# Performance work log

Measured on AMD Instinct MI355X. Metric: run time of the kernel, lower is better.

## Reference

```python
import jax, jax.numpy as jnp
import numpy as np


def setup_inputs() -> dict:
    key = jax.random.key(0)
    k1, k2, k3, k4, k5 = jax.random.split(key, 5)
    B_, S, D_in, D_out, R = 2, 2048, 4096, 4096, 4
    return {
        "x": jax.random.normal(k1, (B_, S, D_in), dtype=jnp.float32),
        "weight": jax.random.normal(k2, (D_out, D_in), dtype=jnp.float32) * 0.02,
        "bias": jax.random.normal(k3, (D_out,), dtype=jnp.float32) * 0.02,
        "scale_A": jax.random.normal(k4, (D_out, R), dtype=jnp.float32),
        "scale_B": jax.random.normal(k5, (R, D_in), dtype=jnp.float32),
        "rank_magnitude": jnp.ones((R,), dtype=jnp.float32),
    }


def reference(x, weight, bias, scale_A, scale_B, rank_magnitude):
    # Factored forward with default bound_mode='tanh', A_max=B_max=1.0, pad=0:
    #   y = sum_k g_k * A[:, k] * ((x * B[k]) @ Q.T) + bias
    Q = weight  # snapped_mode=None, _Q=None -> Q = raw weight
    A = jnp.tanh(scale_A)            # [O, R]
    Bm = jnp.tanh(scale_B)           # [R, I] (pad == 0)
    Ag = A * rank_magnitude[None, :]  # fold g_k into A -> [O, R]
    # [b,s,i] x [r,i] -> [b,s,r,i]; contract i with Q [o,i]; weight by Ag [o,r]
    y = jnp.einsum("bsi,ri,oi,or->bso", x, Bm, Q, Ag)
    return y + bias
```

## Files before the change

kernel.cpp:

```cpp
#include <hip/hip_runtime.h>
#include <hip/hip_bf16.h>

typedef __attribute__((ext_vector_type(8))) short bf16x8;
typedef __attribute__((ext_vector_type(4))) float f32x4;
typedef __attribute__((ext_vector_type(4))) short s16x4;

#define M_DIM 4096
#define N_DIM 4096
#define K_DIM 4096
#define R_DIM 4

__device__ __forceinline__ short to_bf16(float f) {
    __hip_bfloat16 h = __float2bfloat16(f);
    return *reinterpret_cast<short*>(&h);
}

__global__ __launch_bounds__(256)
void k_prep(const float* __restrict__ sA, const float* __restrict__ sB,
            const float* __restrict__ g, float* __restrict__ tB,
            float* __restrict__ tAg) {
    int i = blockIdx.x * 256 + threadIdx.x;
    if (i < R_DIM * K_DIM) {
        tB[i] = tanhf(sB[i]);
    } else {
        int j = i - R_DIM * K_DIM;
        tAg[j] = tanhf(sA[j]) * g[j & 3];
    }
}

__global__ __launch_bounds__(256)
void k_xcast(const float* __restrict__ x, __hip_bfloat16* __restrict__ xb) {
    const size_t i = ((size_t)blockIdx.x * 256 + threadIdx.x) << 3;
    float4 u = *(const float4*)&x[i];
    float4 v = *(const float4*)&x[i + 4];
    bf16x8 pk;
    pk[0] = to_bf16(u.x); pk[1] = to_bf16(u.y);
    pk[2] = to_bf16(u.z); pk[3] = to_bf16(u.w);
    pk[4] = to_bf16(v.x); pk[5] = to_bf16(v.y);
    pk[6] = to_bf16(v.z); pk[7] = to_bf16(v.w);
    *(bf16x8*)&xb[i] = pk;
}

__global__ __launch_bounds__(256)
void k_weff(const float* __restrict__ w, const float* __restrict__ tB,
            const float* __restrict__ tAg, __hip_bfloat16* __restrict__ weff) {
    const int o = blockIdx.x;
    const float a0 = tAg[o * 4 + 0];
    const float a1 = tAg[o * 4 + 1];
    const float a2 = tAg[o * 4 + 2];
    const float a3 = tAg[o * 4 + 3];
#pragma unroll
    for (int it = 0; it < 4; ++it) {
        const int i = (it * 256 + (int)threadIdx.x) << 2;
        float4 wv = *(const float4*)&w[(size_t)o * K_DIM + i];
        float4 b0 = *(const float4*)&tB[0 * K_DIM + i];
        float4 b1 = *(const float4*)&tB[1 * K_DIM + i];
        float4 b2 = *(const float4*)&tB[2 * K_DIM + i];
        float4 b3 = *(const float4*)&tB[3 * K_DIM + i];
        float s0 = a0 * b0.x + a1 * b1.x + a2 * b2.x + a3 * b3.x;
        float s1 = a0 * b0.y + a1 * b1.y + a2 * b2.y + a3 * b3.y;
        float s2 = a0 * b0.z + a1 * b1.z + a2 * b2.z + a3 * b3.z;
        float s3 = a0 * b0.w + a1 * b1.w + a2 * b2.w + a3 * b3.w;
        s16x4 pk;
        pk[0] = to_bf16(wv.x * s0);
        pk[1] = to_bf16(wv.y * s1);
        pk[2] = to_bf16(wv.z * s2);
        pk[3] = to_bf16(wv.w * s3);
        *(s16x4*)&weff[(size_t)o * K_DIM + i] = pk;
    }
}

#define MFMA_N(q, n, bA, bB) \
    acc[2*(q)][(n)]   = __builtin_amdgcn_mfma_f32_16x16x32_bf16(a0, bA, acc[2*(q)][(n)],   0, 0, 0); \
    acc[2*(q)][(n)]   = __builtin_amdgcn_mfma_f32_16x16x32_bf16(a1, bB, acc[2*(q)][(n)],   0, 0, 0); \
    acc[2*(q)+1][(n)] = __builtin_amdgcn_mfma_f32_16x16x32_bf16(a2, bA, acc[2*(q)+1][(n)], 0, 0, 0); \
    acc[2*(q)+1][(n)] = __builtin_amdgcn_mfma_f32_16x16x32_bf16(a3, bB, acc[2*(q)+1][(n)], 0, 0, 0);

#define PHASE(d, q, STAGE_STMT, WAIT_STMT) \
    { \
        const int Ab = ((d) * 2 + wr) * 8192; \
        a0 = FRAG(Ab, (2*(q))   * 16 + l15, cb0); \
        a1 = FRAG(Ab, (2*(q))   * 16 + l15, cb1); \
        a2 = FRAG(Ab, (2*(q)+1) * 16 + l15, cb0); \
        a3 = FRAG(Ab, (2*(q)+1) * 16 + l15, cb1); \
        if ((q) == 0) { \
            const int Bb = 32768 + ((d) * 2 + (wc >> 1)) * 8192; \
            b0 = FRAG(Bb, br0, cb0); b1 = FRAG(Bb, br0, cb1); \
            b2 = FRAG(Bb, br1, cb0); b3 = FRAG(Bb, br1, cb1); \
            b4 = FRAG(Bb, br2, cb0); b5 = FRAG(Bb, br2, cb1); \
            b6 = FRAG(Bb, br3, cb0); b7 = FRAG(Bb, br3, cb1); \
        } \
        STAGE_STMT; \
        __builtin_amdgcn_s_barrier(); \
        asm volatile("s_waitcnt lgkmcnt(0)" ::: "memory"); \
        __builtin_amdgcn_sched_barrier(0); \
        __builtin_amdgcn_s_setprio(1); \
        MFMA_N(q, 0, b0, b1); MFMA_N(q, 1, b2, b3); \
        MFMA_N(q, 2, b4, b5); MFMA_N(q, 3, b6, b7); \
        __builtin_amdgcn_s_setprio(0); \
        WAIT_STMT; \
        __builtin_amdgcn_s_barrier(); \
    }

__global__ __launch_bounds__(512)
void k_gemm8(const __hip_bfloat16* __restrict__ xb,
             const __hip_bfloat16* __restrict__ weff,
             const float* __restrict__ bias, float* __restrict__ out) {
    __shared__ short lds[65536];

    const int tid  = threadIdx.x;
    const int lane = tid & 63;
    const int wid  = tid >> 6;
    const int wr   = wid >> 2;
    const int wc   = wid & 3;
    const int l15  = lane & 15;
    const int cb0  = (lane >> 4) << 4;
    const int cb1  = cb0 + 64;

    const int bid = blockIdx.x;
    const int swz = (bid & 7) * 32 + (bid >> 3);
    const int m0g = (swz >> 4) << 8;
    const int n0g = (swz & 15) << 8;

    const int br0 = (wc & 1) * 64 + 0  + l15;
    const int br1 = (wc & 1) * 64 + 16 + l15;
    const int br2 = (wc & 1) * 64 + 32 + l15;
    const int br3 = (wc & 1) * 64 + 48 + l15;

    auto STAGE = [&](const __hip_bfloat16* __restrict__ src, int gr0, int k0, int base) {
#pragma unroll
        for (int p = 0; p < 2; ++p) {
            const int P    = p * 8192 + tid * 16;
            const int row  = P >> 7;
            const int colb = (P & 127) ^ ((row & 7) << 4);
            const __hip_bfloat16* g = src + ((size_t)(gr0 + row) << 12) + (k0 + (colb >> 1));
            __builtin_amdgcn_global_load_lds(
                (const __attribute__((address_space(1))) void*)g,
                (__attribute__((address_space(3))) void*)&lds[base + (P >> 1)],
                16, 0, 0);
        }
    };

    auto FRAG = [&](int base, int row, int cb) -> bf16x8 {
        const int byte = ((((row << 7) + cb) ^ ((row & 7) << 4))) + base * 2;
        return *(const bf16x8*)((const char*)lds + byte);
    };

    f32x4 acc[8][4] = {};
    bf16x8 a0, a1, a2, a3, b0, b1, b2, b3, b4, b5, b6, b7;

    STAGE(xb,   m0g,       0,  0);
    STAGE(xb,   m0g + 128, 0,  8192);
    STAGE(weff, n0g,       0,  32768);
    STAGE(weff, n0g + 128, 0,  40960);
    STAGE(weff, n0g,       64, 49152);
    STAGE(weff, n0g + 128, 64, 57344);
    asm volatile("s_waitcnt vmcnt(4)" ::: "memory");
    __builtin_amdgcn_s_barrier();

    for (int i = 0; i < 32; ++i) {
        const int t1k = (2 * i + 1) * 64;
        const int kA  = (2 * i + 2 < 64 ? 2 * i + 2 : 63) * 64;
        const int kB  = (2 * i + 3 < 64 ? 2 * i + 3 : 63) * 64;

        PHASE(0, 0, STAGE(xb,   m0g,       t1k, 16384), );
        PHASE(0, 1, STAGE(xb,   m0g + 128, t1k, 24576), );
        PHASE(0, 2, STAGE(weff, n0g,       kA,  32768), );
        PHASE(0, 3, STAGE(weff, n0g + 128, kA,  40960),
              asm volatile("s_waitcnt vmcnt(4)" ::: "memory"));
        PHASE(1, 0, STAGE(xb,   m0g,       kA,  0), );
        PHASE(1, 1, STAGE(xb,   m0g + 128, kA,  8192), );
        PHASE(1, 2, STAGE(weff, n0g,       kB,  49152), );
        PHASE(1, 3, STAGE(weff, n0g + 128, kB,  57344),
              asm volatile("s_waitcnt vmcnt(4)" ::: "memory"));
    }

#pragma unroll
    for (int n = 0; n < 4; ++n) {
        const int col = n0g + wc * 64 + n * 16 + l15;
        const float bv = bias[col];
#pragma unroll
        for (int m = 0; m < 8; ++m) {
            const int rbase = m0g + wr * 128 + m * 16 + ((lane >> 4) << 2);
#pragma unroll
            for (int j = 0; j < 4; ++j)
                out[(size_t)(rbase + j) * N_DIM + col] = acc[m][n][j] + bv;
        }
    }
}

extern "C" void kernel_launch(void* const* d_in, const int* in_sizes, int n_in,
                              void* d_out, int out_size, void* d_ws, size_t ws_size,
                              hipStream_t stream) {
    const float* x    = (const float*)d_in[0];
    const float* w    = (const float*)d_in[1];
    const float* bias = (const float*)d_in[2];
    const float* sA   = (const float*)d_in[3];
    const float* sB   = (const float*)d_in[4];
    const float* g    = (const float*)d_in[5];
    float* out = (float*)d_out;

    __hip_bfloat16* weff = (__hip_bfloat16*)d_ws;
    __hip_bfloat16* xb   = (__hip_bfloat16*)((char*)d_ws + (32ull << 20));
    float* tB  = (float*)((char*)d_ws + (64ull << 20));
    float* tAg = (float*)((char*)d_ws + (64ull << 20) + (R_DIM * K_DIM * 4));

    k_prep<<<dim3((2 * R_DIM * K_DIM) / 256), dim3(256), 0, stream>>>(sA, sB, g, tB, tAg);
    k_xcast<<<dim3((M_DIM * K_DIM) / (256 * 8)), dim3(256), 0, stream>>>(x, xb);
    k_weff<<<dim3(N_DIM), dim3(256), 0, stream>>>(w, tB, tAg, weff);
    k_gemm8<<<dim3((M_DIM / 256) * (N_DIM / 256)), dim3(512), 0, stream>>>(xb, weff, bias, out);
}
```

Baseline: 156.2 us.

## Software-pipeline LDS fragment reads with MFMA using double-buffered A registers

Restructures the GEMM main loop so the A fragments for the next quarter-tile are read from LDS while the current quarter's MFMAs run, alternating between two register sets (x/y). B fragments are read once per half-iteration, and the explicit lgkmcnt waits and per-phase scheduling barriers are dropped so LDS latency can hide behind matrix math. It also adds a min-blocks-per-CU launch bound of 2. That bound tightens the register budget against 128 accumulator registers plus 16 fragment registers, which risks spilling, and LDS use of 128 KB per block may stop two blocks from sharing a CU anyway.

```diff
diff --git a/kernel.cpp b/kernel.cpp
--- a/kernel.cpp
+++ b/kernel.cpp
@@ -70,39 +70,71 @@
     }
 }
 
-#define MFMA_N(q, n, bA, bB) \
-    acc[2*(q)][(n)]   = __builtin_amdgcn_mfma_f32_16x16x32_bf16(a0, bA, acc[2*(q)][(n)],   0, 0, 0); \
-    acc[2*(q)][(n)]   = __builtin_amdgcn_mfma_f32_16x16x32_bf16(a1, bB, acc[2*(q)][(n)],   0, 0, 0); \
-    acc[2*(q)+1][(n)] = __builtin_amdgcn_mfma_f32_16x16x32_bf16(a2, bA, acc[2*(q)+1][(n)], 0, 0, 0); \
-    acc[2*(q)+1][(n)] = __builtin_amdgcn_mfma_f32_16x16x32_bf16(a3, bB, acc[2*(q)+1][(n)], 0, 0, 0);
-
-#define PHASE(d, q, STAGE_STMT, WAIT_STMT) \
-    { \
-        const int Ab = ((d) * 2 + wr) * 8192; \
-        a0 = FRAG(Ab, (2*(q))   * 16 + l15, cb0); \
-        a1 = FRAG(Ab, (2*(q))   * 16 + l15, cb1); \
-        a2 = FRAG(Ab, (2*(q)+1) * 16 + l15, cb0); \
-        a3 = FRAG(Ab, (2*(q)+1) * 16 + l15, cb1); \
-        if ((q) == 0) { \
-            const int Bb = 32768 + ((d) * 2 + (wc >> 1)) * 8192; \
-            b0 = FRAG(Bb, br0, cb0); b1 = FRAG(Bb, br0, cb1); \
-            b2 = FRAG(Bb, br1, cb0); b3 = FRAG(Bb, br1, cb1); \
-            b4 = FRAG(Bb, br2, cb0); b5 = FRAG(Bb, br2, cb1); \
-            b6 = FRAG(Bb, br3, cb0); b7 = FRAG(Bb, br3, cb1); \
-        } \
-        STAGE_STMT; \
-        __builtin_amdgcn_s_barrier(); \
-        asm volatile("s_waitcnt lgkmcnt(0)" ::: "memory"); \
-        __builtin_amdgcn_sched_barrier(0); \
-        __builtin_amdgcn_s_setprio(1); \
-        MFMA_N(q, 0, b0, b1); MFMA_N(q, 1, b2, b3); \
-        MFMA_N(q, 2, b4, b5); MFMA_N(q, 3, b6, b7); \
-        __builtin_amdgcn_s_setprio(0); \
-        WAIT_STMT; \
-        __builtin_amdgcn_s_barrier(); \
-    }
-
-__global__ __launch_bounds__(512)
+#define MFMA(A, B, C) __builtin_amdgcn_mfma_f32_16x16x32_bf16(A, B, C, 0, 0, 0)
+
+#define MFMA_Q(q, A0, A1, A2, A3) \
+    acc[2*(q)][0]   = MFMA(A0, b0, acc[2*(q)][0]); \
+    acc[2*(q)][0]   = MFMA(A1, b1, acc[2*(q)][0]); \
+    acc[2*(q)+1][0] = MFMA(A2, b0, acc[2*(q)+1][0]); \
+    acc[2*(q)+1][0] = MFMA(A3, b1, acc[2*(q)+1][0]); \
+    acc[2*(q)][1]   = MFMA(A0, b2, acc[2*(q)][1]); \
+    acc[2*(q)][1]   = MFMA(A1, b3, acc[2*(q)][1]); \
+    acc[2*(q)+1][1] = MFMA(A2, b2, acc[2*(q)+1][1]); \
+    acc[2*(q)+1][1] = MFMA(A3, b3, acc[2*(q)+1][1]); \
+    acc[2*(q)][2]   = MFMA(A0, b4, acc[2*(q)][2]); \
+    acc[2*(q)][2]   = MFMA(A1, b5, acc[2*(q)][2]); \
+    acc[2*(q)+1][2] = MFMA(A2, b4, acc[2*(q)+1][2]); \
+    acc[2*(q)+1][2] = MFMA(A3, b5, acc[2*(q)+1][2]); \
+    acc[2*(q)][3]   = MFMA(A0, b6, acc[2*(q)][3]); \
+    acc[2*(q)][3]   = MFMA(A1, b7, acc[2*(q)][3]); \
+    acc[2*(q)+1][3] = MFMA(A2, b6, acc[2*(q)+1][3]); \
+    acc[2*(q)+1][3] = MFMA(A3, b7, acc[2*(q)+1][3]);
+
+#define READ_A(d, q, R0, R1, R2, R3) \
+    { const int Ab_ = ((d) * 2 + wr) * 8192; \
+      R0 = FRAG(Ab_, (2*(q))   * 16 + l15, cb0); \
+      R1 = FRAG(Ab_, (2*(q))   * 16 + l15, cb1); \
+      R2 = FRAG(Ab_, (2*(q)+1) * 16 + l15, cb0); \
+      R3 = FRAG(Ab_, (2*(q)+1) * 16 + l15, cb1); }
+
+#define READ_B(d) \
+    { const int Bb_ = 32768 + ((d) * 2 + (wc >> 1)) * 8192; \
+      b0 = FRAG(Bb_, br0, cb0); b1 = FRAG(Bb_, br0, cb1); \
+      b2 = FRAG(Bb_, br1, cb0); b3 = FRAG(Bb_, br1, cb1); \
+      b4 = FRAG(Bb_, br2, cb0); b5 = FRAG(Bb_, br2, cb1); \
+      b6 = FRAG(Bb_, br3, cb0); b7 = FRAG(Bb_, br3, cb1); }
+
+#define PH_FIRST(d, STAGE_STMT) \
+    { STAGE_STMT; \
+      READ_A(d, 0, x0, x1, x2, x3); \
+      READ_B(d); \
+      __builtin_amdgcn_s_barrier(); \
+      __builtin_amdgcn_s_setprio(1); \
+      MFMA_Q(0, x0, x1, x2, x3); \
+      __builtin_amdgcn_s_setprio(0); \
+      READ_A(d, 1, y0, y1, y2, y3); \
+      __builtin_amdgcn_s_barrier(); }
+
+#define PH_MID(d, q, C0, C1, C2, C3, N0, N1, N2, N3, STAGE_STMT) \
+    { STAGE_STMT; \
+      __builtin_amdgcn_s_barrier(); \
+      __builtin_amdgcn_s_setprio(1); \
+      MFMA_Q(q, C0, C1, C2, C3); \
+      __builtin_amdgcn_s_setprio(0); \
+      READ_A(d, (q) + 1, N0, N1, N2, N3); \
+      __builtin_amdgcn_s_barrier(); }
+
+#define PH_LAST(C0, C1, C2, C3, STAGE_STMT) \
+    { STAGE_STMT; \
+      __builtin_amdgcn_s_barrier(); \
+      __builtin_amdgcn_s_setprio(1); \
+      MFMA_Q(3, C0, C1, C2, C3); \
+      __builtin_amdgcn_s_setprio(0); \
+      asm volatile("s_waitcnt vmcnt(4)" ::: "memory"); \
+      __builtin_amdgcn_s_barrier(); \
+      __builtin_amdgcn_sched_barrier(0); }
+
+__global__ __launch_bounds__(512, 2)
 void k_gemm8(const __hip_bfloat16* __restrict__ xb,
              const __hip_bfloat16* __restrict__ weff,
              const float* __restrict__ bias, float* __restrict__ out) {
@@ -147,7 +179,8 @@
     };
 
     f32x4 acc[8][4] = {};
-    bf16x8 a0, a1, a2, a3, b0, b1, b2, b3, b4, b5, b6, b7;
+    bf16x8 x0, x1, x2, x3, y0, y1, y2, y3;
+    bf16x8 b0, b1, b2, b3, b4, b5, b6, b7;
 
     STAGE(xb,   m0g,       0,  0);
     STAGE(xb,   m0g + 128, 0,  8192);
@@ -157,22 +190,21 @@
     STAGE(weff, n0g + 128, 64, 57344);
     asm volatile("s_waitcnt vmcnt(4)" ::: "memory");
     __builtin_amdgcn_s_barrier();
+    __builtin_amdgcn_sched_barrier(0);
 
     for (int i = 0; i < 32; ++i) {
         const int t1k = (2 * i + 1) * 64;
         const int kA  = (2 * i + 2 < 64 ? 2 * i + 2 : 63) * 64;
         const int kB  = (2 * i + 3 < 64 ? 2 * i + 3 : 63) * 64;
 
-        PHASE(0, 0, STAGE(xb,   m0g,       t1k, 16384), );
-        PHASE(0, 1, STAGE(xb,   m0g + 128, t1k, 24576), );
-        PHASE(0, 2, STAGE(weff, n0g,       kA,  32768), );
-        PHASE(0, 3, STAGE(weff, n0g + 128, kA,  40960),
-              asm volatile("s_waitcnt vmcnt(4)" ::: "memory"));
-        PHASE(1, 0, STAGE(xb,   m0g,       kA,  0), );
-        PHASE(1, 1, STAGE(xb,   m0g + 128, kA,  8192), );
-        PHASE(1, 2, STAGE(weff, n0g,       kB,  49152), );
-        PHASE(1, 3, STAGE(weff, n0g + 128, kB,  57344),
-              asm volatile("s_waitcnt vmcnt(4)" ::: "memory"));
+        PH_FIRST(0,                           STAGE(xb,   m0g,       t1k, 16384));
+        PH_MID(0, 1, y0,y1,y2,y3, x0,x1,x2,x3, STAGE(xb,   m0g + 128, t1k, 24576));
+        PH_MID(0, 2, x0,x1,x2,x3, y0,y1,y2,y3, STAGE(weff, n0g,       kA,  32768));
+        PH_LAST(     y0,y1,y2,y3,              STAGE(weff, n0g + 128, kA,  40960));
+        PH_FIRST(1,                           STAGE(xb,   m0g,       kA,  0));
+        PH_MID(1, 1, y0,y1,y2,y3, x0,x1,x2,x3, STAGE(xb,   m0g + 128, kA,  8192));
+        PH_MID(1, 2, x0,x1,x2,x3, y0,y1,y2,y3, STAGE(weff, n0g,       kB,  49152));
+        PH_LAST(     y0,y1,y2,y3,              STAGE(weff, n0g + 128, kB,  57344));
     }
 
 #pragma unroll
```

Result: no change. 159.1 us (+1.8%).

## Reorder GEMM stage schedule and drop second barrier per phase

Applied to the files above, without the earlier changes.

Restructures the 8-phase main loop of the bf16 MFMA GEMM. Each phase now has one barrier instead of two, and the global-to-LDS stage order rotates so the second weff half-tile is loaded one phase later. The vmcnt wait is relaxed from 4 to 2 outstanding loads and moved before the barrier. The aim is to cut synchronisation stalls and keep more loads in flight. The risk is LDS write-after-read hazards if the buffer reuse ordering is not fully covered by the single barrier.

```diff
diff --git a/kernel.cpp b/kernel.cpp
--- a/kernel.cpp
+++ b/kernel.cpp
@@ -76,31 +76,33 @@
     acc[2*(q)+1][(n)] = __builtin_amdgcn_mfma_f32_16x16x32_bf16(a2, bA, acc[2*(q)+1][(n)], 0, 0, 0); \
     acc[2*(q)+1][(n)] = __builtin_amdgcn_mfma_f32_16x16x32_bf16(a3, bB, acc[2*(q)+1][(n)], 0, 0, 0);
 
-#define PHASE(d, q, STAGE_STMT, WAIT_STMT) \
-    { \
-        const int Ab = ((d) * 2 + wr) * 8192; \
-        a0 = FRAG(Ab, (2*(q))   * 16 + l15, cb0); \
-        a1 = FRAG(Ab, (2*(q))   * 16 + l15, cb1); \
-        a2 = FRAG(Ab, (2*(q)+1) * 16 + l15, cb0); \
-        a3 = FRAG(Ab, (2*(q)+1) * 16 + l15, cb1); \
-        if ((q) == 0) { \
-            const int Bb = 32768 + ((d) * 2 + (wc >> 1)) * 8192; \
-            b0 = FRAG(Bb, br0, cb0); b1 = FRAG(Bb, br0, cb1); \
-            b2 = FRAG(Bb, br1, cb0); b3 = FRAG(Bb, br1, cb1); \
-            b4 = FRAG(Bb, br2, cb0); b5 = FRAG(Bb, br2, cb1); \
-            b6 = FRAG(Bb, br3, cb0); b7 = FRAG(Bb, br3, cb1); \
-        } \
-        STAGE_STMT; \
-        __builtin_amdgcn_s_barrier(); \
-        asm volatile("s_waitcnt lgkmcnt(0)" ::: "memory"); \
-        __builtin_amdgcn_sched_barrier(0); \
-        __builtin_amdgcn_s_setprio(1); \
-        MFMA_N(q, 0, b0, b1); MFMA_N(q, 1, b2, b3); \
-        MFMA_N(q, 2, b4, b5); MFMA_N(q, 3, b6, b7); \
-        __builtin_amdgcn_s_setprio(0); \
-        WAIT_STMT; \
-        __builtin_amdgcn_s_barrier(); \
-    }
+#define READ_A(d, q) \
+    { const int Ab_ = ((d) * 2 + wr) * 8192; \
+      a0 = FRAG(Ab_, (2*(q))   * 16 + l15, cb0); \
+      a1 = FRAG(Ab_, (2*(q))   * 16 + l15, cb1); \
+      a2 = FRAG(Ab_, (2*(q)+1) * 16 + l15, cb0); \
+      a3 = FRAG(Ab_, (2*(q)+1) * 16 + l15, cb1); }
+
+#define READ_B(d) \
+    { const int Bb_ = 32768 + ((d) * 2 + (wc >> 1)) * 8192; \
+      b0 = FRAG(Bb_, br0, cb0); b1 = FRAG(Bb_, br0, cb1); \
+      b2 = FRAG(Bb_, br1, cb0); b3 = FRAG(Bb_, br1, cb1); \
+      b4 = FRAG(Bb_, br2, cb0); b5 = FRAG(Bb_, br2, cb1); \
+      b6 = FRAG(Bb_, br3, cb0); b7 = FRAG(Bb_, br3, cb1); }
+
+#define VM2 asm volatile("s_waitcnt vmcnt(2)" ::: "memory")
+
+#define PH(d, q, READS_STMT, STAGE_STMT, VM_STMT) \
+    { READS_STMT; \
+      STAGE_STMT; \
+      VM_STMT; \
+      __builtin_amdgcn_s_barrier(); \
+      asm volatile("s_waitcnt lgkmcnt(0)" ::: "memory"); \
+      __builtin_amdgcn_sched_barrier(0); \
+      __builtin_amdgcn_s_setprio(1); \
+      MFMA_N(q, 0, b0, b1); MFMA_N(q, 1, b2, b3); \
+      MFMA_N(q, 2, b4, b5); MFMA_N(q, 3, b6, b7); \
+      __builtin_amdgcn_s_setprio(0); }
 
 __global__ __launch_bounds__(512)
 void k_gemm8(const __hip_bfloat16* __restrict__ xb,
@@ -149,30 +151,28 @@
     f32x4 acc[8][4] = {};
     bf16x8 a0, a1, a2, a3, b0, b1, b2, b3, b4, b5, b6, b7;
 
+    STAGE(weff, n0g,       0,  32768);
+    STAGE(weff, n0g + 128, 0,  40960);
     STAGE(xb,   m0g,       0,  0);
     STAGE(xb,   m0g + 128, 0,  8192);
-    STAGE(weff, n0g,       0,  32768);
-    STAGE(weff, n0g + 128, 0,  40960);
     STAGE(weff, n0g,       64, 49152);
-    STAGE(weff, n0g + 128, 64, 57344);
-    asm volatile("s_waitcnt vmcnt(4)" ::: "memory");
+    VM2;
     __builtin_amdgcn_s_barrier();
+    __builtin_amdgcn_sched_barrier(0);
 
     for (int i = 0; i < 32; ++i) {
         const int t1k = (2 * i + 1) * 64;
         const int kA  = (2 * i + 2 < 64 ? 2 * i + 2 : 63) * 64;
         const int kB  = (2 * i + 3 < 64 ? 2 * i + 3 : 63) * 64;
 
-        PHASE(0, 0, STAGE(xb,   m0g,       t1k, 16384), );
-        PHASE(0, 1, STAGE(xb,   m0g + 128, t1k, 24576), );
-        PHASE(0, 2, STAGE(weff, n0g,       kA,  32768), );
-        PHASE(0, 3, STAGE(weff, n0g + 128, kA,  40960),
-              asm volatile("s_waitcnt vmcnt(4)" ::: "memory"));
-        PHASE(1, 0, STAGE(xb,   m0g,       kA,  0), );
-        PHASE(1, 1, STAGE(xb,   m0g + 128, kA,  8192), );
-        PHASE(1, 2, STAGE(weff, n0g,       kB,  49152), );
-        PHASE(1, 3, STAGE(weff, n0g + 128, kB,  57344),
-              asm volatile("s_waitcnt vmcnt(4)" ::: "memory"));
+        PH(0, 0, READ_A(0, 0); READ_B(0), STAGE(weff, n0g + 128, t1k, 57344), );
+        PH(0, 1, READ_A(0, 1),            STAGE(xb,   m0g,       t1k, 16384), );
+        PH(0, 2, READ_A(0, 2),            STAGE(xb,   m0g + 128, t1k, 24576), );
+        PH(0, 3, READ_A(0, 3),            STAGE(weff, n0g,       kA,  32768), VM2);
+        PH(1, 0, READ_A(1, 0); READ_B(1), STAGE(weff, n0g + 128, kA,  40960), );
+        PH(1, 1, READ_A(1, 1),            STAGE(xb,   m0g,       kA,  0), );
+        PH(1, 2, READ_A(1, 2),            STAGE(xb,   m0g + 128, kA,  8192), );
+        PH(1, 3, READ_A(1, 3),            STAGE(weff, n0g,       kB,  49152), VM2);
     }
 
 #pragma unroll
```

Measured after the change: 159.8 us. 2.3% more time.
